# Optimization experiments

Hardware: AMD Instinct MI355X
Metric: run time of the kernel (lower is better)

## Reference

```python
import jax, jax.numpy as jnp
import numpy as np

GATE_THRESH = 0.4
LN_EPS = 1e-5
NORM_EPS = 1e-12  # torch F.normalize eps


def setup_inputs() -> dict:
    key = jax.random.key(0)
    ks = jax.random.split(key, 8)
    B, L, H, V = 64, 1024, 64, 32000
    s = lambda k, shape, scale: (jax.random.normal(k, shape, jnp.float32) * scale)
    return {
        "seq": jax.random.randint(ks[0], (B, L), 0, V),
        "embed": s(ks[1], (V, H), 0.02),
        "W1": s(ks[2], (H, 2 * H), 0.05), "b1": jnp.zeros((2 * H,), jnp.float32),
        "W2": s(ks[3], (2 * H, H), 0.05), "b2": jnp.zeros((H,), jnp.float32),
        "gamma": jnp.ones((H,), jnp.float32), "beta": jnp.zeros((H,), jnp.float32),
        "kpW": s(ks[4], (H, H), 0.1),
        "rpW": s(ks[5], (H, H), 0.1), "rpb": jnp.zeros((H,), jnp.float32),
        "outW": s(ks[6], (H, V), 0.05), "outb": jnp.zeros((V,), jnp.float32),
    }


def reference(seq, embed, W1, b1, W2, b2, gamma, beta, kpW, rpW, rpb, outW, outb):
    # embed + FF residual + LayerNorm
    h = embed[seq]                                        # (B,L,H)
    ffo = jax.nn.relu(h @ W1 + b1) @ W2 + b2
    x = h + ffo
    mu = x.mean(-1, keepdims=True)
    var = x.var(-1, keepdims=True)                        # biased, like torch LN
    h = (x - mu) * jax.lax.rsqrt(var + LN_EPS) * gamma + beta

    k_all = h @ kpW                                       # kp projection for all t, (B,L,H)
    B, L, H = h.shape

    def step(M, k):                                       # M: (B,H,H), k: (B,H)
        kn = k / jnp.maximum(jnp.linalg.norm(k, axis=-1, keepdims=True), NORM_EPS)
        vp = jnp.einsum('bij,bj->bi', M, kn)
        err = k - vp
        gate = (jnp.linalg.norm(err, axis=-1) >= GATE_THRESH * jnp.linalg.norm(k, axis=-1)).astype(k.dtype)
        Delta = gate[:, None, None] * err[:, :, None] * kn[:, None, :]
        return M + Delta, None                            # use_ema=False -> plain accumulation

    M0 = jnp.zeros((B, H, H), h.dtype)
    M, _ = jax.lax.scan(step, M0, jnp.swapaxes(k_all[:, :-1], 0, 1))  # scan over L-1 steps

    q = k_all[:, -1]                                      # query from last token
    read = jnp.einsum('bij,bj->bi', M, q)
    return (read @ rpW + rpb) @ outW + outb               # (B,V)
```

## Files before the change

### kernel.cpp

```cpp
#include <hip/hip_runtime.h>
#include <hip/hip_bf16.h>

#define HDIM 64
#define LSEQ 1024
#define NB 64
#define NV 32000
#define CC 32
#define NCH 32
#define NT (NB * LSEQ)

template<int CTRL>
__device__ __forceinline__ float dpp_red(float x) {
  int y = __builtin_amdgcn_update_dpp(0, __float_as_int(x), CTRL, 0xF, 0xF, true);
  return x + __int_as_float(y);
}
__device__ __forceinline__ float quad_sum(float x) {
  x = dpp_red<0xB1>(x);
  x = dpp_red<0x4E>(x);
  return x;
}
__device__ __forceinline__ float wave_sum63(float x) {
  x = dpp_red<0xB1>(x);
  x = dpp_red<0x4E>(x);
  x = dpp_red<0x141>(x);
  x = dpp_red<0x140>(x);
  x = dpp_red<0x142>(x);
  x = dpp_red<0x143>(x);
  return x;
}

__global__ __launch_bounds__(256) void transpose_w(const float* __restrict__ W1,
    const float* __restrict__ kpW, float* __restrict__ W1T, float* __restrict__ kpWT)
{
  const int tid = blockIdx.x * 256 + threadIdx.x;
  if (tid < 8192) { const int c = tid >> 6, j = tid & 63; W1T[tid] = W1[j * 128 + c]; }
  else { const int e = tid - 8192; const int i = e >> 6, j = e & 63; kpWT[e] = kpW[j * 64 + i]; }
}

__global__ __launch_bounds__(256, 1) void tok4(
    const int* __restrict__ seq, const float* __restrict__ embed,
    const float* __restrict__ W1T, const float* __restrict__ b1,
    const float* __restrict__ W2, const float* __restrict__ b2,
    const float* __restrict__ gamma, const float* __restrict__ beta,
    const float* __restrict__ kpWT, float* __restrict__ kallT,
    float* __restrict__ thr2_all, float* __restrict__ inv_all)
{
  const int tok = blockIdx.x * 256 + threadIdx.x;
  const int row = seq[tok];
  float h[64], x[64];
  const float4* ep = (const float4*)(embed + (size_t)row * HDIM);
  #pragma unroll
  for (int q = 0; q < 16; ++q) {
    const float4 v = ep[q];
    h[4*q] = v.x; h[4*q+1] = v.y; h[4*q+2] = v.z; h[4*q+3] = v.w;
  }
  #pragma unroll
  for (int j = 0; j < 64; ++j) x[j] = h[j] + b2[j];

  for (int c = 0; c < 128; ++c) {
    const float* w1r = W1T + c * 64;
    float a0 = 0.f, a1 = 0.f, a2 = 0.f, a3 = 0.f;
    #pragma unroll
    for (int j = 0; j < 64; j += 4) {
      a0 = fmaf(h[j],   w1r[j],   a0);
      a1 = fmaf(h[j+1], w1r[j+1], a1);
      a2 = fmaf(h[j+2], w1r[j+2], a2);
      a3 = fmaf(h[j+3], w1r[j+3], a3);
    }
    const float y = fmaxf(b1[c] + ((a0 + a1) + (a2 + a3)), 0.f);
    const float* w2r = W2 + c * 64;
    #pragma unroll
    for (int j = 0; j < 64; ++j) x[j] = fmaf(y, w2r[j], x[j]);
  }

  float s0=0.f,s1=0.f,s2=0.f,s3=0.f,q0=0.f,q1=0.f,q2=0.f,q3=0.f;
  #pragma unroll
  for (int j = 0; j < 64; j += 4) {
    s0 += x[j]; s1 += x[j+1]; s2 += x[j+2]; s3 += x[j+3];
    q0 = fmaf(x[j],   x[j],   q0); q1 = fmaf(x[j+1], x[j+1], q1);
    q2 = fmaf(x[j+2], x[j+2], q2); q3 = fmaf(x[j+3], x[j+3], q3);
  }
  const float mu  = ((s0+s1)+(s2+s3)) * (1.f/64.f);
  const float var = ((q0+q1)+(q2+q3)) * (1.f/64.f) - mu * mu;
  const float rs  = rsqrtf(var + 1e-5f);
  #pragma unroll
  for (int j = 0; j < 64; ++j) h[j] = (x[j] - mu) * rs * gamma[j] + beta[j];

  float nk2 = 0.f;
  for (int i = 0; i < 64; ++i) {
    const float* kr = kpWT + i * 64;
    float c0=0.f,c1=0.f,c2=0.f,c3=0.f;
    #pragma unroll
    for (int j = 0; j < 64; j += 4) {
      c0 = fmaf(h[j],   kr[j],   c0);
      c1 = fmaf(h[j+1], kr[j+1], c1);
      c2 = fmaf(h[j+2], kr[j+2], c2);
      c3 = fmaf(h[j+3], kr[j+3], c3);
    }
    const float ki = (c0 + c1) + (c2 + c3);
    nk2 = fmaf(ki, ki, nk2);
    kallT[(size_t)i * NT + tok] = ki;
  }
  thr2_all[tok] = 0.16f * nk2;
  inv_all[tok]  = 1.f / fmaxf(sqrtf(nk2), 1e-12f);
}

__global__ __launch_bounds__(64) void gram2(const float* __restrict__ kallT,
    const float* __restrict__ inv_all, float* __restrict__ Gg)
{
  const int bi = blockIdx.x;
  const int b = bi >> 5, ch = bi & 31;
  const int l = threadIdx.x;
  const int t0 = (l & 7) * 4, s0 = (l >> 3) * 4;
  const size_t gb = (size_t)b * LSEQ + ch * CC;
  float g00=0,g01=0,g02=0,g03=0, g10=0,g11=0,g12=0,g13=0;
  float g20=0,g21=0,g22=0,g23=0, g30=0,g31=0,g32=0,g33=0;
  for (int j = 0; j < 64; ++j) {
    const float* rowp = kallT + (size_t)j * NT + gb;
    const float4 a = *(const float4*)(rowp + t0);
    const float4 c = *(const float4*)(rowp + s0);
    g00=fmaf(a.x,c.x,g00); g01=fmaf(a.x,c.y,g01); g02=fmaf(a.x,c.z,g02); g03=fmaf(a.x,c.w,g03);
    g10=fmaf(a.y,c.x,g10); g11=fmaf(a.y,c.y,g11); g12=fmaf(a.y,c.z,g12); g13=fmaf(a.y,c.w,g13);
    g20=fmaf(a.z,c.x,g20); g21=fmaf(a.z,c.y,g21); g22=fmaf(a.z,c.z,g22); g23=fmaf(a.z,c.w,g23);
    g30=fmaf(a.w,c.x,g30); g31=fmaf(a.w,c.y,g31); g32=fmaf(a.w,c.z,g32); g33=fmaf(a.w,c.w,g33);
  }
  const float4 it = *(const float4*)(inv_all + gb + t0);
  const float4 is = *(const float4*)(inv_all + gb + s0);
  float* Go = Gg + (size_t)bi * (CC * CC);
  float4 o;
  o.x=g00*it.x*is.x; o.y=g01*it.x*is.y; o.z=g02*it.x*is.z; o.w=g03*it.x*is.w;
  *(float4*)(Go + (t0+0)*CC + s0) = o;
  o.x=g10*it.y*is.x; o.y=g11*it.y*is.y; o.z=g12*it.y*is.z; o.w=g13*it.y*is.w;
  *(float4*)(Go + (t0+1)*CC + s0) = o;
  o.x=g20*it.z*is.x; o.y=g21*it.z*is.y; o.z=g22*it.z*is.z; o.w=g23*it.z*is.w;
  *(float4*)(Go + (t0+2)*CC + s0) = o;
  o.x=g30*it.w*is.x; o.y=g31*it.w*is.y; o.z=g32*it.w*is.z; o.w=g33*it.w*is.w;
  *(float4*)(Go + (t0+3)*CC + s0) = o;
}

__global__ __launch_bounds__(192, 1) void scan6(
    const float* __restrict__ kallT, const float* __restrict__ thr2_all,
    const float* __restrict__ inv_all, const float* __restrict__ Gg,
    float* __restrict__ readv)
{
  __shared__ float kS[3][CC * 68];
  __shared__ float GS[2][CC * CC];
  __shared__ float rS[CC * 64];
  __shared__ float cstS[CC * 64];
  __shared__ float thr2S[2][CC];
  __shared__ float invS[3][CC];

  const int b = blockIdx.x, tid = threadIdx.x;
  const int w = tid >> 6, l = tid & 63;
  const int A = l >> 2, B4 = l & 3;
  const int r0 = 32 * (w - 1) + 2 * A;
  const int jb = 16 * B4;
  const size_t gbase = (size_t)b * LSEQ;

  float M0[16], M1[16], acc[32];
  #pragma unroll
  for (int q = 0; q < 16; ++q) { M0[q] = 0.f; M1[q] = 0.f; }

#define A2_RUN16(KB, IB, T0) do {                                              \
    const float* kr0_ = &kS[KB][(T0) * 68 + jb];                               \
    float4 kA0 = ((const float4*)kr0_)[0], kA1 = ((const float4*)kr0_)[1],     \
           kA2 = ((const float4*)kr0_)[2], kA3 = ((const float4*)kr0_)[3];     \
    float  ivA = invS[IB][(T0)];                                               \
    float4 kB0, kB1, kB2, kB3; float ivB = 0.f;                                \
    _Pragma("unroll")                                                          \
    for (int i = 0; i < 16; ++i) {                                             \
      const int t = (T0) + i;                                                  \
      if (i < 15) {                                                            \
        const float* knx_ = &kS[KB][(t + 1) * 68 + jb];                        \
        if ((i & 1) == 0) {                                                    \
          kB0 = ((const float4*)knx_)[0]; kB1 = ((const float4*)knx_)[1];      \
          kB2 = ((const float4*)knx_)[2]; kB3 = ((const float4*)knx_)[3];      \
          ivB = invS[IB][t + 1];                                               \
        } else {                                                               \
          kA0 = ((const float4*)knx_)[0]; kA1 = ((const float4*)knx_)[1];      \
          kA2 = ((const float4*)knx_)[2]; kA3 = ((const float4*)knx_)[3];      \
          ivA = invS[IB][t + 1];                                               \
        }                                                                      \
      }                                                                        \
      float4 kq[4]; float iv;                                                  \
      if ((i & 1) == 0) { kq[0]=kA0; kq[1]=kA1; kq[2]=kA2; kq[3]=kA3; iv=ivA; }\
      else              { kq[0]=kB0; kq[1]=kB1; kq[2]=kB2; kq[3]=kB3; iv=ivB; }\
      float p0a=0.f,p0b=0.f,p1a=0.f,p1b=0.f;                                   \
      _Pragma("unroll")                                                        \
      for (int q2 = 0; q2 < 4; ++q2) {                                         \
        const float4 kv = kq[q2];                                              \
        p0a = fmaf(M0[4*q2+0], kv.x, p0a); p0b = fmaf(M0[4*q2+1], kv.y, p0b);  \
        p0a = fmaf(M0[4*q2+2], kv.z, p0a); p0b = fmaf(M0[4*q2+3], kv.w, p0b);  \
        p1a = fmaf(M1[4*q2+0], kv.x, p1a); p1b = fmaf(M1[4*q2+1], kv.y, p1b);  \
        p1a = fmaf(M1[4*q2+2], kv.z, p1a); p1b = fmaf(M1[4*q2+3], kv.w, p1b);  \
      }                                                                        \
      float p0 = quad_sum(p0a + p0b);                                          \
      float p1 = quad_sum(p1a + p1b);                                          \
      if (B4 == 0) *(float2*)&rS[t * 64 + r0] = make_float2(p0 * iv, p1 * iv); \
    }                                                                          \
  } while (0)

#define C_RUN16(KB, IB, S0) do {                                               \
    const float* kr0_ = &kS[KB][(S0) * 68 + jb];                               \
    float4 kA0 = ((const float4*)kr0_)[0], kA1 = ((const float4*)kr0_)[1],     \
           kA2 = ((const float4*)kr0_)[2], kA3 = ((const float4*)kr0_)[3];     \
    float2 cA  = *(const float2*)&cstS[(S0) * 64 + r0];                        \
    float  ivA = invS[IB][(S0)];                                               \
    float4 kB0, kB1, kB2, kB3; float2 cB = make_float2(0.f, 0.f); float ivB = 0.f; \
    _Pragma("unroll")                                                          \
    for (int i = 0; i < 16; ++i) {                                             \
      const int s = (S0) + i;                                                  \
      if (i < 15) {                                                            \
        const float* knx_ = &kS[KB][(s + 1) * 68 + jb];                        \
        if ((i & 1) == 0) {                                                    \
          kB0 = ((const float4*)knx_)[0]; kB1 = ((const float4*)knx_)[1];      \
          kB2 = ((const float4*)knx_)[2]; kB3 = ((const float4*)knx_)[3];      \
          cB  = *(const float2*)&cstS[(s + 1) * 64 + r0];                      \
          ivB = invS[IB][s + 1];                                               \
        } else {                                                               \
          kA0 = ((const float4*)knx_)[0]; kA1 = ((const float4*)knx_)[1];      \
          kA2 = ((const float4*)knx_)[2]; kA3 = ((const float4*)knx_)[3];      \
          cA  = *(const float2*)&cstS[(s + 1) * 64 + r0];                      \
          ivA = invS[IB][s + 1];                                               \
        }                                                                      \
      }                                                                        \
      float4 kq[4]; float2 cc2; float iv;                                      \
      if ((i & 1) == 0) { kq[0]=kA0; kq[1]=kA1; kq[2]=kA2; kq[3]=kA3; cc2=cA; iv=ivA; } \
      else              { kq[0]=kB0; kq[1]=kB1; kq[2]=kB2; kq[3]=kB3; cc2=cB; iv=ivB; } \
      const float c0 = cc2.x * iv, c1 = cc2.y * iv;                            \
      _Pragma("unroll")                                                        \
      for (int q2 = 0; q2 < 4; ++q2) {                                         \
        const float4 kv = kq[q2];                                              \
        M0[4*q2+0] = fmaf(c0, kv.x, M0[4*q2+0]); M0[4*q2+1] = fmaf(c0, kv.y, M0[4*q2+1]); \
        M0[4*q2+2] = fmaf(c0, kv.z, M0[4*q2+2]); M0[4*q2+3] = fmaf(c0, kv.w, M0[4*q2+3]); \
        M1[4*q2+0] = fmaf(c1, kv.x, M1[4*q2+0]); M1[4*q2+1] = fmaf(c1, kv.y, M1[4*q2+1]); \
        M1[4*q2+2] = fmaf(c1, kv.z, M1[4*q2+2]); M1[4*q2+3] = fmaf(c1, kv.w, M1[4*q2+3]); \
      }                                                                        \
    }                                                                          \
  } while (0)

#define B_SLICE(Q, CBUF, CGI, LASTCH) do {                                     \
    const int t0_ = 8 * (Q);                                                   \
    float kr_[8], rr_[8];                                                      \
    _Pragma("unroll")                                                          \
    for (int i = 0; i < 8; ++i) {                                              \
      kr_[i] = kS[CBUF][(t0_ + i) * 68 + l];                                   \
      rr_[i] = rS[(t0_ + i) * 64 + l];                                         \
    }                                                                          \
    const float4 tha = ((const float4*)&thr2S[CGI][t0_])[0];                   \
    const float4 thb = ((const float4*)&thr2S[CGI][t0_])[1];                   \
    const float th8[8] = {tha.x,tha.y,tha.z,tha.w, thb.x,thb.y,thb.z,thb.w};   \
    float g2_[2][32];                                                          \
    _Pragma("unroll")                                                          \
    for (int q = (t0_ + 1) >> 2; q < 8; ++q) {                                 \
      const float4 v = ((const float4*)&GS[CGI][t0_ * 32])[q];                 \
      g2_[0][4*q+0] = v.x; g2_[0][4*q+1] = v.y;                                \
      g2_[0][4*q+2] = v.z; g2_[0][4*q+3] = v.w;                                \
    }                                                                          \
    float err_ = acc[t0_] + kr_[0] - rr_[0];                                   \
    float red_ = wave_sum63(err_ * err_);                                      \
    _Pragma("unroll")                                                          \
    for (int i = 0; i < 8; ++i) {                                              \
      const int t = t0_ + i;                                                   \
      if (i < 7) {                                                             \
        _Pragma("unroll")                                                      \
        for (int q = (t + 2) >> 2; q < 8; ++q) {                               \
          const float4 v = ((const float4*)&GS[CGI][(t + 1) * 32])[q];         \
          g2_[(i+1)&1][4*q+0] = v.x; g2_[(i+1)&1][4*q+1] = v.y;                \
          g2_[(i+1)&1][4*q+2] = v.z; g2_[(i+1)&1][4*q+3] = v.w;                \
        }                                                                      \
      }                                                                        \
      const float ne2_ = __int_as_float(                                       \
          __builtin_amdgcn_readlane(__float_as_int(red_), 63));                \
      bool gate_ = (ne2_ >= th8[i]);                                           \
      if ((LASTCH) && t == CC - 1) gate_ = false;                              \
      const float c = gate_ ? err_ : 0.f;                                      \
      cstS[t * 64 + l] = c;                                                    \
      if (i < 7) {                                                             \
        acc[t + 1] = fmaf(-g2_[i & 1][t + 1], c, acc[t + 1]);                  \
        err_ = acc[t + 1] + kr_[i + 1] - rr_[i + 1];                           \
        red_ = wave_sum63(err_ * err_);                                        \
      }                                                                        \
      _Pragma("unroll")                                                        \
      for (int u = (i < 7) ? (t + 2) : (t + 1); u < CC; ++u)                   \
        acc[u] = fmaf(-g2_[i & 1][u], c, acc[u]);                              \
    }                                                                          \
  } while (0)

  if (w < 2) {
    const float* src = kallT + (size_t)l * NT + gbase + w * 16;
    float4 v[4];
    #pragma unroll
    for (int q = 0; q < 4; ++q) v[q] = ((const float4*)src)[q];
    #pragma unroll
    for (int q = 0; q < 4; ++q) {
      const int t0 = w * 16 + q * 4;
      kS[0][(t0+0)*68 + l] = v[q].x; kS[0][(t0+1)*68 + l] = v[q].y;
      kS[0][(t0+2)*68 + l] = v[q].z; kS[0][(t0+3)*68 + l] = v[q].w;
    }
  } else {
    const float4* gsrc = (const float4*)(Gg + (size_t)b * NCH * (CC * CC));
    float4 g[4];
    #pragma unroll
    for (int q = 0; q < 4; ++q) g[q] = gsrc[q * 64 + l];
    #pragma unroll
    for (int q = 0; q < 4; ++q) ((float4*)GS[0])[q * 64 + l] = g[q];
    if (l < CC) thr2S[0][l] = thr2_all[gbase + l];
    else        invS[0][l - CC] = inv_all[gbase + (l - CC)];
  }
  __syncthreads();

  for (int ch = 0; ch < NCH; ++ch) {
    const int cb = ch % 3, pb = (ch + 2) % 3, nb = (ch + 1) % 3;
    const int cg = ch & 1, ng = 1 - cg;
    const bool lastch = (ch == NCH - 1);

    if (w == 0) {
      #pragma unroll
      for (int u = 0; u < 32; ++u) acc[u] = 0.f;
      if (!lastch) {
        const float* src = kallT + (size_t)l * NT + gbase + (ch + 1) * CC;
        float4 v[8];
        #pragma unroll
        for (int q = 0; q < 8; ++q) v[q] = ((const float4*)src)[q];
        #pragma unroll
        for (int q = 0; q < 8; ++q) {
          const int t0 = q * 4;
          kS[nb][(t0+0)*68 + l] = v[q].x; kS[nb][(t0+1)*68 + l] = v[q].y;
          kS[nb][(t0+2)*68 + l] = v[q].z; kS[nb][(t0+3)*68 + l] = v[q].w;
        }
        const float4* gsrc = (const float4*)(Gg + ((size_t)b * NCH + ch + 1) * (CC * CC));
        float4 g[4];
        #pragma unroll
        for (int q = 0; q < 4; ++q) g[q] = gsrc[q * 64 + l];
        #pragma unroll
        for (int q = 0; q < 4; ++q) ((float4*)GS[ng])[q * 64 + l] = g[q];
        if (l < CC) thr2S[ng][l] = thr2_all[gbase + (ch + 1) * CC + l];
        else        invS[nb][l - CC] = inv_all[gbase + (ch + 1) * CC + (l - CC)];
      }
    } else {
      if (ch > 0) C_RUN16(pb, pb, 16);
      A2_RUN16(cb, cb, 0);
    }
    __syncthreads();

    if (w == 0) { B_SLICE(0, cb, cg, lastch); B_SLICE(1, cb, cg, lastch); }
    else        A2_RUN16(cb, cb, 16);
    __syncthreads();

    if (w == 0) { B_SLICE(2, cb, cg, lastch); B_SLICE(3, cb, cg, lastch); }
    else        C_RUN16(cb, cb, 0);
    __syncthreads();
  }

  {
    constexpr int fb = (NCH - 1) % 3;
    if (w > 0) {
      C_RUN16(fb, fb, 16);
      const float* kr = &kS[fb][(CC - 1) * 68 + jb];
      float p0a=0.f,p0b=0.f,p1a=0.f,p1b=0.f;
      #pragma unroll
      for (int q2 = 0; q2 < 4; ++q2) {
        const float4 kv = ((const float4*)kr)[q2];
        p0a = fmaf(M0[4*q2+0], kv.x, p0a); p0b = fmaf(M0[4*q2+1], kv.y, p0b);
        p0a = fmaf(M0[4*q2+2], kv.z, p0a); p0b = fmaf(M0[4*q2+3], kv.w, p0b);
        p1a = fmaf(M1[4*q2+0], kv.x, p1a); p1b = fmaf(M1[4*q2+1], kv.y, p1b);
        p1a = fmaf(M1[4*q2+2], kv.z, p1a); p1b = fmaf(M1[4*q2+3], kv.w, p1b);
      }
      float d0 = quad_sum(p0a + p0b);
      float d1 = quad_sum(p1a + p1b);
      if (B4 == 0) *(float2*)&readv[b * 64 + r0] = make_float2(d0, d1);
    }
  }
#undef A2_RUN16
#undef C_RUN16
#undef B_SLICE
}

__global__ __launch_bounds__(64) void rproj_kernel(const float* __restrict__ readv,
    const float* __restrict__ rpW, const float* __restrict__ rpb, float* __restrict__ r2T)
{
  const int b = blockIdx.x, i = threadIdx.x;
  const float* rv = readv + b * 64;
  float acc = rpb[i];
  #pragma unroll
  for (int j = 0; j < 64; ++j)
    acc = fmaf(rv[j], rpW[j * 64 + i], acc);
  r2T[i * 64 + b] = acc;
}

__global__ __launch_bounds__(128, 1) void out_kernel(const float* __restrict__ r2T,
    const float* __restrict__ outW, const float* __restrict__ outb,
    float* __restrict__ out)
{
  const int v = blockIdx.x * 128 + threadIdx.x;
  float acc[64];
  #pragma unroll
  for (int b = 0; b < 64; ++b) acc[b] = 0.f;
  for (int k = 0; k < 64; ++k) {
    const float wv = outW[(size_t)k * NV + v];
    const float* rr = r2T + k * 64;
    #pragma unroll
    for (int b = 0; b < 64; ++b)
      acc[b] = fmaf(rr[b], wv, acc[b]);
  }
  const float ob = outb[v];
  #pragma unroll
  for (int b = 0; b < 64; ++b)
    out[(size_t)b * NV + v] = acc[b] + ob;
}

extern "C" void kernel_launch(void* const* d_in, const int* in_sizes, int n_in,
                              void* d_out, int out_size, void* d_ws, size_t ws_size,
                              hipStream_t stream)
{
  const int*   seq   = (const int*)d_in[0];
  const float* embed = (const float*)d_in[1];
  const float* W1    = (const float*)d_in[2];
  const float* b1    = (const float*)d_in[3];
  const float* W2    = (const float*)d_in[4];
  const float* b2    = (const float*)d_in[5];
  const float* gam   = (const float*)d_in[6];
  const float* bet   = (const float*)d_in[7];
  const float* kpW   = (const float*)d_in[8];
  const float* rpW   = (const float*)d_in[9];
  const float* rpb   = (const float*)d_in[10];
  const float* outW  = (const float*)d_in[11];
  const float* outb  = (const float*)d_in[12];
  float* out = (float*)d_out;

  float* ws = (float*)d_ws;
  float* kallT = ws;
  float* G     = kallT + (size_t)HDIM * NT;
  float* thr2  = G     + (size_t)NB * NCH * CC * CC;
  float* inv   = thr2  + NT;
  float* readv = inv   + NT;
  float* r2T   = readv + NB * HDIM;
  float* W1T   = r2T   + NB * HDIM;
  float* kpWT  = W1T   + 8192;

  hipLaunchKernelGGL(transpose_w, dim3(48), dim3(256), 0, stream, W1, kpW, W1T, kpWT);
  hipLaunchKernelGGL(tok4, dim3(256), dim3(256), 0, stream,
                     seq, embed, W1T, b1, W2, b2, gam, bet, kpWT, kallT, thr2, inv);
  hipLaunchKernelGGL(gram2, dim3(NB * NCH), dim3(64), 0, stream, kallT, inv, G);
  hipLaunchKernelGGL(scan6, dim3(NB), dim3(192), 0, stream, kallT, thr2, inv, G, readv);
  hipLaunchKernelGGL(rproj_kernel, dim3(NB), dim3(64), 0, stream, readv, rpW, rpb, r2T);
  hipLaunchKernelGGL(out_kernel, dim3(NV / 128), dim3(128), 0, stream, r2T, outW, outb, out);
}
```

Measured before the change: 461.4 us.

## Split scan A-phase across replicated wave groups and offload prefetch to dedicated wave

The scan kernel grows from 3 to 8 waves. Waves 1-6 form three replicated groups, each holding a full copy of the M state. The per-chunk A2 projections are split by time range across these groups, so the two A2 phases fold into one. A separate wave 7 now handles the global prefetch of the next chunk's keys, Gram block and scalars, which frees wave 0 to work only on the B slices. The aim is to shorten the serial per-chunk critical path, at the cost of redundant C-phase work in every group and higher register and occupancy pressure.

Measured after the change: 484.4 us. +5.0%, slower.

```diff
diff --git a/kernel.cpp b/kernel.cpp
--- a/kernel.cpp
+++ b/kernel.cpp
@@ -138,7 +138,7 @@
   *(float4*)(Go + (t0+3)*CC + s0) = o;
 }
 
-__global__ __launch_bounds__(192, 1) void scan6(
+__global__ __launch_bounds__(512, 1) void scan6(
     const float* __restrict__ kallT, const float* __restrict__ thr2_all,
     const float* __restrict__ inv_all, const float* __restrict__ Gg,
     float* __restrict__ readv)
@@ -153,7 +153,10 @@
   const int b = blockIdx.x, tid = threadIdx.x;
   const int w = tid >> 6, l = tid & 63;
   const int A = l >> 2, B4 = l & 3;
-  const int r0 = 32 * (w - 1) + 2 * A;
+  const int hw = w - 1;
+  const int tm = hw >> 1;
+  const int half = hw & 1;
+  const int r0 = 32 * half + 2 * A;
   const int jb = 16 * B4;
   const size_t gbase = (size_t)b * LSEQ;
 
@@ -161,16 +164,16 @@
   #pragma unroll
   for (int q = 0; q < 16; ++q) { M0[q] = 0.f; M1[q] = 0.f; }
 
-#define A2_RUN16(KB, IB, T0) do {                                              \
+#define A2_RUN(KB, IB, T0, TN) do {                                            \
     const float* kr0_ = &kS[KB][(T0) * 68 + jb];                               \
     float4 kA0 = ((const float4*)kr0_)[0], kA1 = ((const float4*)kr0_)[1],     \
            kA2 = ((const float4*)kr0_)[2], kA3 = ((const float4*)kr0_)[3];     \
     float  ivA = invS[IB][(T0)];                                               \
     float4 kB0, kB1, kB2, kB3; float ivB = 0.f;                                \
     _Pragma("unroll")                                                          \
-    for (int i = 0; i < 16; ++i) {                                             \
+    for (int i = 0; i < (TN) - (T0); ++i) {                                    \
       const int t = (T0) + i;                                                  \
-      if (i < 15) {                                                            \
+      if (i < (TN) - (T0) - 1) {                                               \
         const float* knx_ = &kS[KB][(t + 1) * 68 + jb];                        \
         if ((i & 1) == 0) {                                                    \
           kB0 = ((const float4*)knx_)[0]; kB1 = ((const float4*)knx_)[1];      \
@@ -200,7 +203,7 @@
     }                                                                          \
   } while (0)
 
-#define C_RUN16(KB, IB, S0) do {                                               \
+#define C_RUN(KB, IB, S0, SN) do {                                             \
     const float* kr0_ = &kS[KB][(S0) * 68 + jb];                               \
     float4 kA0 = ((const float4*)kr0_)[0], kA1 = ((const float4*)kr0_)[1],     \
            kA2 = ((const float4*)kr0_)[2], kA3 = ((const float4*)kr0_)[3];     \
@@ -208,9 +211,9 @@
     float  ivA = invS[IB][(S0)];                                               \
     float4 kB0, kB1, kB2, kB3; float2 cB = make_float2(0.f, 0.f); float ivB = 0.f; \
     _Pragma("unroll")                                                          \
-    for (int i = 0; i < 16; ++i) {                                             \
+    for (int i = 0; i < (SN) - (S0); ++i) {                                    \
       const int s = (S0) + i;                                                  \
-      if (i < 15) {                                                            \
+      if (i < (SN) - (S0) - 1) {                                               \
         const float* knx_ = &kS[KB][(s + 1) * 68 + jb];                        \
         if ((i & 1) == 0) {                                                    \
           kB0 = ((const float4*)knx_)[0]; kB1 = ((const float4*)knx_)[1];      \
@@ -298,7 +301,7 @@
       kS[0][(t0+0)*68 + l] = v[q].x; kS[0][(t0+1)*68 + l] = v[q].y;
       kS[0][(t0+2)*68 + l] = v[q].z; kS[0][(t0+3)*68 + l] = v[q].w;
     }
-  } else {
+  } else if (w == 2) {
     const float4* gsrc = (const float4*)(Gg + (size_t)b * NCH * (CC * CC));
     float4 g[4];
     #pragma unroll
@@ -318,45 +321,46 @@
     if (w == 0) {
       #pragma unroll
       for (int u = 0; u < 32; ++u) acc[u] = 0.f;
-      if (!lastch) {
-        const float* src = kallT + (size_t)l * NT + gbase + (ch + 1) * CC;
-        float4 v[8];
-        #pragma unroll
-        for (int q = 0; q < 8; ++q) v[q] = ((const float4*)src)[q];
-        #pragma unroll
-        for (int q = 0; q < 8; ++q) {
-          const int t0 = q * 4;
-          kS[nb][(t0+0)*68 + l] = v[q].x; kS[nb][(t0+1)*68 + l] = v[q].y;
-          kS[nb][(t0+2)*68 + l] = v[q].z; kS[nb][(t0+3)*68 + l] = v[q].w;
-        }
-        const float4* gsrc = (const float4*)(Gg + ((size_t)b * NCH + ch + 1) * (CC * CC));
-        float4 g[4];
-        #pragma unroll
-        for (int q = 0; q < 4; ++q) g[q] = gsrc[q * 64 + l];
-        #pragma unroll
-        for (int q = 0; q < 4; ++q) ((float4*)GS[ng])[q * 64 + l] = g[q];
-        if (l < CC) thr2S[ng][l] = thr2_all[gbase + (ch + 1) * CC + l];
-        else        invS[nb][l - CC] = inv_all[gbase + (ch + 1) * CC + (l - CC)];
+    } else if (w <= 6) {
+      if (ch > 0) C_RUN(pb, pb, 16, 32);
+      if (tm == 0)      A2_RUN(cb, cb, 0, 11);
+      else if (tm == 1) A2_RUN(cb, cb, 11, 21);
+      else              A2_RUN(cb, cb, 21, 32);
+    }
+    __syncthreads();
+
+    if (w == 0) { B_SLICE(0, cb, cg, lastch); B_SLICE(1, cb, cg, lastch); }
+    else if (w == 7 && !lastch) {
+      const float* src = kallT + (size_t)l * NT + gbase + (ch + 1) * CC;
+      float4 v[8];
+      #pragma unroll
+      for (int q = 0; q < 8; ++q) v[q] = ((const float4*)src)[q];
+      #pragma unroll
+      for (int q = 0; q < 8; ++q) {
+        const int t0 = q * 4;
+        kS[nb][(t0+0)*68 + l] = v[q].x; kS[nb][(t0+1)*68 + l] = v[q].y;
+        kS[nb][(t0+2)*68 + l] = v[q].z; kS[nb][(t0+3)*68 + l] = v[q].w;
       }
-    } else {
-      if (ch > 0) C_RUN16(pb, pb, 16);
-      A2_RUN16(cb, cb, 0);
+      const float4* gsrc = (const float4*)(Gg + ((size_t)b * NCH + ch + 1) * (CC * CC));
+      float4 g[4];
+      #pragma unroll
+      for (int q = 0; q < 4; ++q) g[q] = gsrc[q * 64 + l];
+      #pragma unroll
+      for (int q = 0; q < 4; ++q) ((float4*)GS[ng])[q * 64 + l] = g[q];
+      if (l < CC) thr2S[ng][l] = thr2_all[gbase + (ch + 1) * CC + l];
+      else        invS[nb][l - CC] = inv_all[gbase + (ch + 1) * CC + (l - CC)];
     }
     __syncthreads();
 
-    if (w == 0) { B_SLICE(0, cb, cg, lastch); B_SLICE(1, cb, cg, lastch); }
-    else        A2_RUN16(cb, cb, 16);
-    __syncthreads();
-
     if (w == 0) { B_SLICE(2, cb, cg, lastch); B_SLICE(3, cb, cg, lastch); }
-    else        C_RUN16(cb, cb, 0);
+    else if (w <= 6) C_RUN(cb, cb, 0, 16);
     __syncthreads();
   }
 
   {
     constexpr int fb = (NCH - 1) % 3;
-    if (w > 0) {
-      C_RUN16(fb, fb, 16);
+    if (w >= 1 && w <= 2) {
+      C_RUN(fb, fb, 16, 32);
       const float* kr = &kS[fb][(CC - 1) * 68 + jb];
       float p0a=0.f,p0b=0.f,p1a=0.f,p1b=0.f;
       #pragma unroll
@@ -372,8 +376,8 @@
       if (B4 == 0) *(float2*)&readv[b * 64 + r0] = make_float2(d0, d1);
     }
   }
-#undef A2_RUN16
-#undef C_RUN16
+#undef A2_RUN
+#undef C_RUN
 #undef B_SLICE
 }
 
@@ -443,7 +447,7 @@
   hipLaunchKernelGGL(tok4, dim3(256), dim3(256), 0, stream,
                      seq, embed, W1T, b1, W2, b2, gam, bet, kpWT, kallT, thr2, inv);
   hipLaunchKernelGGL(gram2, dim3(NB * NCH), dim3(64), 0, stream, kallT, inv, G);
-  hipLaunchKernelGGL(scan6, dim3(NB), dim3(192), 0, stream, kallT, thr2, inv, G, readv);
+  hipLaunchKernelGGL(scan6, dim3(NB), dim3(512), 0, stream, kallT, thr2, inv, G, readv);
   hipLaunchKernelGGL(rproj_kernel, dim3(NB), dim3(64), 0, stream, readv, rpW, rpb, r2T);
   hipLaunchKernelGGL(out_kernel, dim3(NV / 128), dim3(128), 0, stream, r2T, outW, outb, out);
 }
```
